# Kernel tuning notes

Measured on AMD Instinct MI355X. Metric: run time of the kernel, lower is better.

The kernel has to match this reference:

```python
import jax, jax.numpy as jnp
import numpy as np

N = 100_000
E = 1_600_000
D_IN, D_H, D_L = 128, 64, 32


def _glorot(key, shape):
    fan_in, fan_out = shape[0], shape[1]
    s = jnp.sqrt(6.0 / (fan_in + fan_out)).astype(jnp.float32)
    return jax.random.uniform(key, shape, jnp.float32, -s, s)


def setup_inputs() -> dict:
    key = jax.random.key(0)
    ks = jax.random.split(key, 8)
    x = jax.random.normal(ks[0], (N, D_IN), jnp.float32)
    edge_index = jax.random.randint(ks[1], (2, E), 0, N, dtype=jnp.int64)
    return {
        "x": x,
        "edge_index": edge_index,
        "W1": _glorot(ks[2], (D_IN, D_H)),
        "b1": jnp.zeros((D_H,), jnp.float32),
        "W2": _glorot(ks[3], (D_H, D_L)),
        "b2": jnp.zeros((D_L,), jnp.float32),
        "Wd1": _glorot(ks[4], (D_L, D_H)),
        "bd1": jnp.zeros((D_H,), jnp.float32),
        "Wd2": _glorot(ks[5], (D_H, D_IN)),
        "bd2": jnp.zeros((D_IN,), jnp.float32),
    }


def gcn_conv(x, W, b, src, dst, num_nodes):
    """PyG GCNConv: add self-loops, symmetric normalization, aggregate, bias."""
    loop = jnp.arange(num_nodes, dtype=src.dtype)
    s = jnp.concatenate([src, loop])  # sources (message senders)
    d = jnp.concatenate([dst, loop])  # targets (message receivers)
    deg = jax.ops.segment_sum(jnp.ones_like(s, dtype=x.dtype), d, num_segments=num_nodes)
    dinv = jnp.where(deg > 0, jax.lax.rsqrt(deg), 0.0)
    norm = dinv[s] * dinv[d]                      # [E+N]
    h = x @ W                                     # [N, out] dense transform first
    msgs = h[s] * norm[:, None]                   # gather + scale, [E+N, out]
    out = jax.ops.segment_sum(msgs, d, num_segments=num_nodes)  # scatter-add
    return out + b


def reference(x, edge_index, W1, b1, W2, b2, Wd1, bd1, Wd2, bd2):
    src, dst = edge_index[0], edge_index[1]
    n = x.shape[0]
    z = gcn_conv(x, W1, b1, src, dst, n)
    z = jax.nn.relu(z)
    z = gcn_conv(z, W2, b2, src, dst, n)          # latent embedding
    h = jax.nn.relu(z @ Wd1 + bd1)
    reconstructed_x = h @ Wd2 + bd2
    return (reconstructed_x, z)
```

## Files before the change

kernel.cpp:

```cpp
#include <hip/hip_runtime.h>
#include <stdint.h>

#define N_NODES 100000
#define N_EDGES 1600000
#define D_INF   128
#define D_HID   64
#define D_LAT   32
#define NB      98

typedef __attribute__((ext_vector_type(8))) short bf16x8;
typedef __attribute__((ext_vector_type(4))) float f32x4;

__device__ __forceinline__ unsigned short f2bf(float v) {
  union { float f; unsigned int u; } x; x.f = v;
  unsigned int u = x.u + 0x7FFF + ((x.u >> 16) & 1);
  return (unsigned short)(u >> 16);
}
__device__ __forceinline__ float bf2f(unsigned short h) {
  union { unsigned int u; float f; } x; x.u = ((unsigned int)h) << 16;
  return x.f;
}


#define NBKT      196
#define BKT_SHIFT 9
#define BKT_CAP   10240
#define EPB       4096
#define ABLOCKS   391
#define SPLITB    4

__global__ void k_zerobkt(int* __restrict__ bkcnt) {
  int t = threadIdx.x;
  if (t < NBKT) bkcnt[t] = 0;
}

__global__ __launch_bounds__(256) void k_binA(const int* __restrict__ esrc,
                                              const int* __restrict__ edst,
                                              int* __restrict__ bkcnt,
                                              int2* __restrict__ stage) {
  __shared__ int cnt[NBKT];
  __shared__ int sc[256];
  __shared__ int garel[NBKT];
  __shared__ int pos[NBKT];
  __shared__ __align__(16) int2 stg[EPB];
  __shared__ int gaddr[EPB];
  int t = threadIdx.x;
  int e0 = blockIdx.x * EPB;

  for (int i = t; i < NBKT; i += 256) cnt[i] = 0;
  __syncthreads();

  int ds[16], ss[16];
  const int4* s4 = (const int4*)esrc;
  const int4* d4 = (const int4*)edst;
#pragma unroll
  for (int i = 0; i < 4; i++) {
    int idx4 = (e0 >> 2) + i * 256 + t;
    int4 dd = make_int4(-1, -1, -1, -1);
    int4 sv = make_int4(0, 0, 0, 0);
    if (idx4 < N_EDGES / 4) { dd = d4[idx4]; sv = s4[idx4]; }
    ds[i*4+0] = dd.x; ds[i*4+1] = dd.y; ds[i*4+2] = dd.z; ds[i*4+3] = dd.w;
    ss[i*4+0] = sv.x; ss[i*4+1] = sv.y; ss[i*4+2] = sv.z; ss[i*4+3] = sv.w;
  }
#pragma unroll
  for (int j = 0; j < 16; j++)
    if (ds[j] >= 0) atomicAdd(&cnt[ds[j] >> BKT_SHIFT], 1);
  __syncthreads();

  int c = (t < NBKT) ? cnt[t] : 0;
  sc[t] = c;
  __syncthreads();
  int incl = c;
#pragma unroll
  for (int off = 1; off < 256; off <<= 1) {
    int x = (t >= off) ? sc[t - off] : 0;
    __syncthreads();
    incl += x;
    sc[t] = incl;
    __syncthreads();
  }
  if (t < NBKT) {
    int lb = incl - c;
    int gb = 0;
    if (c > 0) gb = t * BKT_CAP + atomicAdd(&bkcnt[t], c);
    garel[t] = gb - lb;
    pos[t]   = lb;
  }
  __syncthreads();

#pragma unroll
  for (int j = 0; j < 16; j++) {
    if (ds[j] >= 0) {
      int b  = ds[j] >> BKT_SHIFT;
      int lp = atomicAdd(&pos[b], 1);
      stg[lp]   = make_int2(ss[j], ds[j]);
      gaddr[lp] = garel[b] + lp;
    }
  }
  __syncthreads();

  int nval = N_EDGES - e0; if (nval > EPB) nval = EPB;
  for (int i = t; i < nval; i += 256)
    stage[gaddr[i]] = stg[i];
}

__global__ __launch_bounds__(256) void k_countB(const int2* __restrict__ stage,
                                                const int* __restrict__ bkcnt,
                                                int* __restrict__ counts) {
  __shared__ int hist[1 << BKT_SHIFT];
  int b = blockIdx.x;
  int t = threadIdx.x;
  for (int i = t; i < (1 << BKT_SHIFT); i += 256) hist[i] = 0;
  __syncthreads();
  int n = bkcnt[b];
  int nlo = b << BKT_SHIFT;
  const int2* reg = stage + (size_t)b * BKT_CAP;
  for (int i = t; i < n; i += 256)
    atomicAdd(&hist[reg[i].y - nlo], 1);
  __syncthreads();
  for (int i = t; i < (1 << BKT_SHIFT); i += 256) {
    int node = nlo + i;
    if (node < N_NODES) counts[node] = hist[i];
  }
}

__global__ void k_blocksum(const int* __restrict__ counts, int* __restrict__ bsums) {
  __shared__ int red[4];
  int base = blockIdx.x * 1024 + threadIdx.x * 4;
  int s = 0;
#pragma unroll
  for (int j = 0; j < 4; j++) { int i = base + j; if (i < N_NODES) s += counts[i]; }
#pragma unroll
  for (int off = 32; off > 0; off >>= 1) s += __shfl_down(s, off, 64);
  if ((threadIdx.x & 63) == 0) red[threadIdx.x >> 6] = s;
  __syncthreads();
  if (threadIdx.x == 0) bsums[blockIdx.x] = red[0] + red[1] + red[2] + red[3];
}

__global__ void k_scanblocks(const int* __restrict__ bsums, int* __restrict__ bbase,
                             int* __restrict__ offsets) {
  __shared__ int sh[128];
  int t = threadIdx.x;
  int v = (t < NB) ? bsums[t] : 0;
  sh[t] = v;
  __syncthreads();
  int incl = v;
#pragma unroll
  for (int off = 1; off < 128; off <<= 1) {
    int x = (t >= off) ? sh[t - off] : 0;
    __syncthreads();
    incl += x;
    sh[t] = incl;
    __syncthreads();
  }
  if (t < NB) bbase[t] = incl - v;
  if (t == NB - 1) offsets[N_NODES] = incl;
}

__global__ void k_scanchunk(const int* __restrict__ counts, const int* __restrict__ bbase,
                            int* __restrict__ offsets, int* __restrict__ cursor,
                            float* __restrict__ dinv) {
  __shared__ int sh[256];
  int b = blockIdx.x, t = threadIdx.x;
  int base = b * 1024 + t * 4;
  int v[4]; int s = 0;
#pragma unroll
  for (int j = 0; j < 4; j++) { v[j] = (base + j < N_NODES) ? counts[base + j] : 0; s += v[j]; }
  sh[t] = s;
  __syncthreads();
  int incl = s;
#pragma unroll
  for (int off = 1; off < 256; off <<= 1) {
    int x = (t >= off) ? sh[t - off] : 0;
    __syncthreads();
    incl += x;
    sh[t] = incl;
    __syncthreads();
  }
  int run = bbase[b] + incl - s;
#pragma unroll
  for (int j = 0; j < 4; j++) {
    int i = base + j;
    if (i < N_NODES) {
      offsets[i] = run;
      cursor[i]  = run;
      dinv[i]    = rsqrtf((float)(v[j] + 1));
      run += v[j];
    }
  }
}

__global__ __launch_bounds__(256) void k_binB(const int2* __restrict__ stage,
                                              const int* __restrict__ bkcnt,
                                              int* __restrict__ cursor,
                                              const float* __restrict__ dinv,
                                              int2* __restrict__ csr8) {
  int b   = blockIdx.x / SPLITB;
  int sub = blockIdx.x % SPLITB;
  int n = bkcnt[b];
  const int2* reg = stage + (size_t)b * BKT_CAP;
  for (int i = sub * 256 + threadIdx.x; i < n; i += SPLITB * 256) {
    int2 e = reg[i];
    int slot = atomicAdd(&cursor[e.y], 1);
    float w = dinv[e.x] * dinv[e.y];
    csr8[slot] = make_int2(e.x, __float_as_int(w));
  }
}


__global__ void k_prep_w(const float* __restrict__ W1, const float* __restrict__ W2,
                         const float* __restrict__ Wd1, const float* __restrict__ Wd2,
                         unsigned short* __restrict__ w1hi, unsigned short* __restrict__ w1lo,
                         unsigned short* __restrict__ w2hi, unsigned short* __restrict__ w2lo,
                         unsigned short* __restrict__ wd1hi, unsigned short* __restrict__ wd1lo,
                         unsigned short* __restrict__ wd2hi, unsigned short* __restrict__ wd2lo) {
  const float* src; unsigned short *hi, *lo; int K, M;
  switch (blockIdx.x) {
    case 0:  src = W1;  hi = w1hi;  lo = w1lo;  K = 128; M = 64;  break;
    case 1:  src = W2;  hi = w2hi;  lo = w2lo;  K = 64;  M = 32;  break;
    case 2:  src = Wd1; hi = wd1hi; lo = wd1lo; K = 32;  M = 64;  break;
    default: src = Wd2; hi = wd2hi; lo = wd2lo; K = 64;  M = 128; break;
  }
  int KP = K + 8;
  for (int i = threadIdx.x; i < K * M; i += 256) {
    int k = i / M, c = i % M;
    float v = src[i];
    unsigned short h = f2bf(v);
    hi[c * KP + k] = h;
    lo[c * KP + k] = f2bf(v - bf2f(h));
  }
}


template<int NODES, int K, int M>
__global__ __launch_bounds__(256) void k_mfma_gemm(const float* __restrict__ X,
                                                   const unsigned short* __restrict__ Bhi,
                                                   const unsigned short* __restrict__ Blo,
                                                   unsigned short* __restrict__ Y16) {
  constexpr int KP     = K + 8;
  constexpr int NSTRIP = M / 16;
  constexpr int KSTEPS = K / 32;
  constexpr int MTW    = (NODES / 16) * NSTRIP / 4;
  __shared__ __align__(16) unsigned short Ahi[NODES * KP];
  __shared__ __align__(16) unsigned short Alo[NODES * KP];

  int t = threadIdx.x;
  int node0 = blockIdx.x * NODES;

  for (int i = t; i < NODES * K / 4; i += 256) {
    int n = i / (K / 4), f4 = i % (K / 4);
    float4 v = make_float4(0.f, 0.f, 0.f, 0.f);
    if (node0 + n < N_NODES) v = ((const float4*)(X + (size_t)(node0 + n) * K))[f4];
    int base = n * KP + f4 * 4;
    float vv[4] = {v.x, v.y, v.z, v.w};
#pragma unroll
    for (int j = 0; j < 4; j++) {
      unsigned short h = f2bf(vv[j]);
      Ahi[base + j] = h;
      Alo[base + j] = f2bf(vv[j] - bf2f(h));
    }
  }
  __syncthreads();

  int w = t >> 6, lane = t & 63;
  int quad = lane >> 4, r16 = lane & 15;
  int strip = w % NSTRIP;

  bf16x8 bh[KSTEPS], bl[KSTEPS];
  const unsigned short* bp = Bhi + (strip * 16 + r16) * KP + quad * 8;
  const unsigned short* bq = Blo + (strip * 16 + r16) * KP + quad * 8;
#pragma unroll
  for (int ks = 0; ks < KSTEPS; ks++) {
    bh[ks] = *(const bf16x8*)(bp + ks * 32);
    bl[ks] = *(const bf16x8*)(bq + ks * 32);
  }

#pragma unroll
  for (int c = 0; c < MTW; c++) {
    int mt = (w / NSTRIP) * MTW + c;
    f32x4 acc = {0.f, 0.f, 0.f, 0.f};
    const unsigned short* ap = &Ahi[(mt * 16 + r16) * KP + quad * 8];
    const unsigned short* aq = &Alo[(mt * 16 + r16) * KP + quad * 8];
#pragma unroll
    for (int ks = 0; ks < KSTEPS; ks++) {
      bf16x8 ah = *(const bf16x8*)(ap + ks * 32);
      bf16x8 al = *(const bf16x8*)(aq + ks * 32);
      acc = __builtin_amdgcn_mfma_f32_16x16x32_bf16(ah, bh[ks], acc, 0, 0, 0);
      acc = __builtin_amdgcn_mfma_f32_16x16x32_bf16(ah, bl[ks], acc, 0, 0, 0);
      acc = __builtin_amdgcn_mfma_f32_16x16x32_bf16(al, bh[ks], acc, 0, 0, 0);
    }
    int gn  = node0 + mt * 16 + quad * 4;
    int col = strip * 16 + r16;
#pragma unroll
    for (int r = 0; r < 4; r++) {
      if (gn + r < N_NODES) Y16[(size_t)(gn + r) * M + col] = f2bf(acc[r]);
    }
  }
}


template<int FEAT, bool RELU>
__global__ __launch_bounds__(256) void k_aggregate(const unsigned short* __restrict__ H16,
                            const int* __restrict__ offsets,
                            const int2* __restrict__ csr8,
                            const float* __restrict__ dinv, const float* __restrict__ bias,
                            float* __restrict__ OUT) {
  constexpr int LPG    = FEAT / 4;
  constexpr int GROUPS = 64 / LPG;

  int node = blockIdx.x * 4 + (threadIdx.x >> 6);
  int lane = threadIdx.x & 63;
  if (node >= N_NODES) return;
  int beg = offsets[node], end = offsets[node + 1];
  int g  = lane / LPG;
  int f4 = lane % LPG;

  float a0 = 0.f, a1 = 0.f, a2 = 0.f, a3 = 0.f;

  int p = beg;
  for (; p + 2 * GROUPS <= end; p += 2 * GROUPS) {
    int2 e0 = csr8[p + g];
    int2 e1 = csr8[p + GROUPS + g];
    ushort4 h0 = *(const ushort4*)(H16 + (size_t)e0.x * FEAT + f4 * 4);
    ushort4 h1 = *(const ushort4*)(H16 + (size_t)e1.x * FEAT + f4 * 4);
    float w0 = __int_as_float(e0.y), w1 = __int_as_float(e1.y);
    a0 += bf2f(h0.x) * w0; a1 += bf2f(h0.y) * w0;
    a2 += bf2f(h0.z) * w0; a3 += bf2f(h0.w) * w0;
    a0 += bf2f(h1.x) * w1; a1 += bf2f(h1.y) * w1;
    a2 += bf2f(h1.z) * w1; a3 += bf2f(h1.w) * w1;
  }
  for (; p < end; p += GROUPS) {
    int q = p + g;
    int2 e = (q < end) ? csr8[q] : make_int2(node, 0);
    ushort4 h = *(const ushort4*)(H16 + (size_t)e.x * FEAT + f4 * 4);
    float w = __int_as_float(e.y);
    a0 += bf2f(h.x) * w; a1 += bf2f(h.y) * w;
    a2 += bf2f(h.z) * w; a3 += bf2f(h.w) * w;
  }

#pragma unroll
  for (int off = LPG; off < 64; off <<= 1) {
    a0 += __shfl_xor(a0, off, 64);
    a1 += __shfl_xor(a1, off, 64);
    a2 += __shfl_xor(a2, off, 64);
    a3 += __shfl_xor(a3, off, 64);
  }

  if (g == 0) {
    float di = dinv[node];
    float sw = di * di;
    ushort4 hs = *(const ushort4*)(H16 + (size_t)node * FEAT + f4 * 4);
    float4 bv = *(const float4*)(bias + f4 * 4);
    a0 += bf2f(hs.x) * sw + bv.x;
    a1 += bf2f(hs.y) * sw + bv.y;
    a2 += bf2f(hs.z) * sw + bv.z;
    a3 += bf2f(hs.w) * sw + bv.w;
    if (RELU) {
      a0 = fmaxf(a0, 0.f); a1 = fmaxf(a1, 0.f);
      a2 = fmaxf(a2, 0.f); a3 = fmaxf(a3, 0.f);
    }
    float4 o; o.x = a0; o.y = a1; o.z = a2; o.w = a3;
    *(float4*)(OUT + (size_t)node * FEAT + f4 * 4) = o;
  }
}


__global__ __launch_bounds__(256) void k_decoder_mfma(
    const float* __restrict__ Z,
    const unsigned short* __restrict__ B1hi, const unsigned short* __restrict__ B1lo,
    const float* __restrict__ bd1,
    const unsigned short* __restrict__ B2hi, const unsigned short* __restrict__ B2lo,
    const float* __restrict__ bd2, float* __restrict__ RECON) {
  constexpr int KP1 = 40;
  constexpr int KP2 = 72;
  __shared__ __align__(16) unsigned short Azhi[64 * KP1];
  __shared__ __align__(16) unsigned short Azlo[64 * KP1];
  __shared__ __align__(16) unsigned short H3hi[64 * KP2];
  __shared__ __align__(16) unsigned short H3lo[64 * KP2];
  int t = threadIdx.x;
  int node0 = blockIdx.x * 64;

  for (int i = t; i < 512; i += 256) {
    int n = i >> 3, f4 = i & 7;
    float4 v = make_float4(0.f, 0.f, 0.f, 0.f);
    if (node0 + n < N_NODES) v = ((const float4*)(Z + (size_t)(node0 + n) * 32))[f4];
    int base = n * KP1 + f4 * 4;
    float vv[4] = {v.x, v.y, v.z, v.w};
#pragma unroll
    for (int j = 0; j < 4; j++) {
      unsigned short h = f2bf(vv[j]);
      Azhi[base + j] = h;
      Azlo[base + j] = f2bf(vv[j] - bf2f(h));
    }
  }
  __syncthreads();

  int w = t >> 6, lane = t & 63;
  int quad = lane >> 4, r16 = lane & 15;

  {
    int col = w * 16 + r16;
    float bias1 = bd1[col];
    bf16x8 bh = *(const bf16x8*)(B1hi + col * KP1 + quad * 8);
    bf16x8 bl = *(const bf16x8*)(B1lo + col * KP1 + quad * 8);
#pragma unroll
    for (int m = 0; m < 4; m++) {
      bf16x8 ah = *(const bf16x8*)(Azhi + (m * 16 + r16) * KP1 + quad * 8);
      bf16x8 al = *(const bf16x8*)(Azlo + (m * 16 + r16) * KP1 + quad * 8);
      f32x4 acc = {0.f, 0.f, 0.f, 0.f};
      acc = __builtin_amdgcn_mfma_f32_16x16x32_bf16(ah, bh, acc, 0, 0, 0);
      acc = __builtin_amdgcn_mfma_f32_16x16x32_bf16(ah, bl, acc, 0, 0, 0);
      acc = __builtin_amdgcn_mfma_f32_16x16x32_bf16(al, bh, acc, 0, 0, 0);
#pragma unroll
      for (int r = 0; r < 4; r++) {
        int row = m * 16 + quad * 4 + r;
        float hv = fmaxf(acc[r] + bias1, 0.f);
        unsigned short h = f2bf(hv);
        H3hi[row * KP2 + col] = h;
        H3lo[row * KP2 + col] = f2bf(hv - bf2f(h));
      }
    }
  }
  __syncthreads();

#pragma unroll
  for (int sp = 0; sp < 2; sp++) {
    int strip = w + sp * 4;
    int col = strip * 16 + r16;
    float bias2 = bd2[col];
    const unsigned short* b2h = B2hi + col * KP2 + quad * 8;
    const unsigned short* b2l = B2lo + col * KP2 + quad * 8;
    bf16x8 bh0 = *(const bf16x8*)(b2h);
    bf16x8 bh1 = *(const bf16x8*)(b2h + 32);
    bf16x8 bl0 = *(const bf16x8*)(b2l);
    bf16x8 bl1 = *(const bf16x8*)(b2l + 32);
#pragma unroll
    for (int m = 0; m < 4; m++) {
      const unsigned short* ahp = H3hi + (m * 16 + r16) * KP2 + quad * 8;
      const unsigned short* alp = H3lo + (m * 16 + r16) * KP2 + quad * 8;
      bf16x8 ah0 = *(const bf16x8*)(ahp);
      bf16x8 ah1 = *(const bf16x8*)(ahp + 32);
      bf16x8 al0 = *(const bf16x8*)(alp);
      bf16x8 al1 = *(const bf16x8*)(alp + 32);
      f32x4 acc = {0.f, 0.f, 0.f, 0.f};
      acc = __builtin_amdgcn_mfma_f32_16x16x32_bf16(ah0, bh0, acc, 0, 0, 0);
      acc = __builtin_amdgcn_mfma_f32_16x16x32_bf16(ah1, bh1, acc, 0, 0, 0);
      acc = __builtin_amdgcn_mfma_f32_16x16x32_bf16(ah0, bl0, acc, 0, 0, 0);
      acc = __builtin_amdgcn_mfma_f32_16x16x32_bf16(ah1, bl1, acc, 0, 0, 0);
      acc = __builtin_amdgcn_mfma_f32_16x16x32_bf16(al0, bh0, acc, 0, 0, 0);
      acc = __builtin_amdgcn_mfma_f32_16x16x32_bf16(al1, bh1, acc, 0, 0, 0);
#pragma unroll
      for (int r = 0; r < 4; r++) {
        int n = node0 + m * 16 + quad * 4 + r;
        if (n < N_NODES) RECON[(size_t)n * 128 + col] = acc[r] + bias2;
      }
    }
  }
}


extern "C" void kernel_launch(void* const* d_in, const int* in_sizes, int n_in,
                              void* d_out, int out_size, void* d_ws, size_t ws_size,
                              hipStream_t stream) {
  const float* x    = (const float*)d_in[0];
  const int*   eidx = (const int*)d_in[1];
  const int*   esrc = eidx;
  const int*   edst = eidx + N_EDGES;
  const float* W1  = (const float*)d_in[2];
  const float* b1  = (const float*)d_in[3];
  const float* W2  = (const float*)d_in[4];
  const float* b2  = (const float*)d_in[5];
  const float* Wd1 = (const float*)d_in[6];
  const float* bd1 = (const float*)d_in[7];
  const float* Wd2 = (const float*)d_in[8];
  const float* bd2 = (const float*)d_in[9];

  float* recon = (float*)d_out;
  float* z     = (float*)d_out + (size_t)N_NODES * D_INF;
  int2*           stage = (int2*)recon;
  unsigned short* h1_16 = (unsigned short*)recon;
  float*          z1    = (float*)((char*)recon + 12800000);
  unsigned short* h2_16 = (unsigned short*)((char*)recon + 38400000);

  char* ws = (char*)d_ws;
  int*   counts  = (int*)(ws + 0);
  int*   offsets = (int*)(ws + 409600);
  int*   cursor  = (int*)(ws + 819200);
  float* dinv    = (float*)(ws + 1228800);
  int*   bsums   = (int*)(ws + 1638400);
  int*   bbase   = (int*)(ws + 1639424);
  int2*  csr8    = (int2*)(ws + 1640448);
  unsigned short* w1hi  = (unsigned short*)(ws + 14440448);
  unsigned short* w1lo  = (unsigned short*)(ws + 14457856);
  unsigned short* w2hi  = (unsigned short*)(ws + 14475264);
  unsigned short* w2lo  = (unsigned short*)(ws + 14479872);
  unsigned short* wd1hi = (unsigned short*)(ws + 14484480);
  unsigned short* wd1lo = (unsigned short*)(ws + 14489600);
  unsigned short* wd2hi = (unsigned short*)(ws + 14494720);
  unsigned short* wd2lo = (unsigned short*)(ws + 14513152);
  int*   bkcnt  = (int*)(ws + 14531584);

  k_zerobkt<<<1, 256, 0, stream>>>(bkcnt);
  k_binA<<<ABLOCKS, 256, 0, stream>>>(esrc, edst, bkcnt, stage);
  k_countB<<<NBKT, 256, 0, stream>>>(stage, bkcnt, counts);
  k_blocksum<<<NB, 256, 0, stream>>>(counts, bsums);
  k_scanblocks<<<1, 128, 0, stream>>>(bsums, bbase, offsets);
  k_scanchunk<<<NB, 256, 0, stream>>>(counts, bbase, offsets, cursor, dinv);
  k_binB<<<NBKT * SPLITB, 256, 0, stream>>>(stage, bkcnt, cursor, dinv, csr8);
  k_prep_w<<<4, 256, 0, stream>>>(W1, W2, Wd1, Wd2, w1hi, w1lo, w2hi, w2lo,
                                  wd1hi, wd1lo, wd2hi, wd2lo);

  k_mfma_gemm<64, 128, 64><<<(N_NODES + 63) / 64, 256, 0, stream>>>(x, w1hi, w1lo, h1_16);
  k_aggregate<64, true><<<(N_NODES + 3) / 4, 256, 0, stream>>>(h1_16, offsets, csr8, dinv, b1, z1);
  k_mfma_gemm<64, 64, 32><<<(N_NODES + 63) / 64, 256, 0, stream>>>(z1, w2hi, w2lo, h2_16);
  k_aggregate<32, false><<<(N_NODES + 3) / 4, 256, 0, stream>>>(h2_16, offsets, csr8, dinv, b2, z);
  k_decoder_mfma<<<(N_NODES + 63) / 64, 256, 0, stream>>>(z, wd1hi, wd1lo, bd1,
                                                          wd2hi, wd2lo, bd2, recon);
}
```

Baseline: 344.8 us.

## Split degree counting across blocks and widen aggregate loads to 8 bf16

```diff
diff --git a/kernel.cpp b/kernel.cpp
--- a/kernel.cpp
+++ b/kernel.cpp
@@ -10,6 +10,7 @@
 
 typedef __attribute__((ext_vector_type(8))) short bf16x8;
 typedef __attribute__((ext_vector_type(4))) float f32x4;
+typedef __attribute__((ext_vector_type(8))) unsigned short u16x8;
 
 __device__ __forceinline__ unsigned short f2bf(float v) {
   union { float f; unsigned int u; } x; x.f = v;
@@ -28,10 +29,12 @@
 #define EPB       4096
 #define ABLOCKS   391
 #define SPLITB    4
-
-__global__ void k_zerobkt(int* __restrict__ bkcnt) {
-  int t = threadIdx.x;
-  if (t < NBKT) bkcnt[t] = 0;
+#define SPLITC    4
+
+__global__ void k_zeroinit(int* __restrict__ counts, int* __restrict__ bkcnt) {
+  int i = blockIdx.x * 256 + threadIdx.x;
+  if (i < N_NODES) counts[i] = 0;
+  if (blockIdx.x == 0 && threadIdx.x < NBKT) bkcnt[threadIdx.x] = 0;
 }
 
 __global__ __launch_bounds__(256) void k_binA(const int* __restrict__ esrc,
@@ -108,19 +111,23 @@
                                                 const int* __restrict__ bkcnt,
                                                 int* __restrict__ counts) {
   __shared__ int hist[1 << BKT_SHIFT];
-  int b = blockIdx.x;
+  int b   = blockIdx.x / SPLITC;
+  int sub = blockIdx.x % SPLITC;
   int t = threadIdx.x;
   for (int i = t; i < (1 << BKT_SHIFT); i += 256) hist[i] = 0;
   __syncthreads();
   int n = bkcnt[b];
   int nlo = b << BKT_SHIFT;
   const int2* reg = stage + (size_t)b * BKT_CAP;
-  for (int i = t; i < n; i += 256)
+  for (int i = sub * 256 + t; i < n; i += SPLITC * 256)
     atomicAdd(&hist[reg[i].y - nlo], 1);
   __syncthreads();
   for (int i = t; i < (1 << BKT_SHIFT); i += 256) {
     int node = nlo + i;
-    if (node < N_NODES) counts[node] = hist[i];
+    if (node < N_NODES) {
+      int v = hist[i];
+      if (v) atomicAdd(&counts[node], v);
+    }
   }
 }
 
@@ -305,62 +312,71 @@
                             const int2* __restrict__ csr8,
                             const float* __restrict__ dinv, const float* __restrict__ bias,
                             float* __restrict__ OUT) {
-  constexpr int LPG    = FEAT / 4;
-  constexpr int GROUPS = 64 / LPG;
+  constexpr int LPE    = FEAT / 8;
+  constexpr int GROUPS = 64 / LPE;
 
   int node = blockIdx.x * 4 + (threadIdx.x >> 6);
   int lane = threadIdx.x & 63;
   if (node >= N_NODES) return;
   int beg = offsets[node], end = offsets[node + 1];
-  int g  = lane / LPG;
-  int f4 = lane % LPG;
-
-  float a0 = 0.f, a1 = 0.f, a2 = 0.f, a3 = 0.f;
-
-  int p = beg;
-  for (; p + 2 * GROUPS <= end; p += 2 * GROUPS) {
-    int2 e0 = csr8[p + g];
-    int2 e1 = csr8[p + GROUPS + g];
-    ushort4 h0 = *(const ushort4*)(H16 + (size_t)e0.x * FEAT + f4 * 4);
-    ushort4 h1 = *(const ushort4*)(H16 + (size_t)e1.x * FEAT + f4 * 4);
+  int g  = lane / LPE;
+  int f8 = lane % LPE;
+
+  float a0=0.f,a1=0.f,a2=0.f,a3=0.f,a4=0.f,a5=0.f,a6=0.f,a7=0.f;
+
+  for (int p = beg; p < end; p += 2 * GROUPS) {
+    int q0 = p + g, q1 = p + GROUPS + g;
+    int2 e0 = (q0 < end) ? csr8[q0] : make_int2(node, 0);
+    int2 e1 = (q1 < end) ? csr8[q1] : make_int2(node, 0);
+    u16x8 h0 = *(const u16x8*)(H16 + (size_t)e0.x * FEAT + f8 * 8);
+    u16x8 h1 = *(const u16x8*)(H16 + (size_t)e1.x * FEAT + f8 * 8);
     float w0 = __int_as_float(e0.y), w1 = __int_as_float(e1.y);
-    a0 += bf2f(h0.x) * w0; a1 += bf2f(h0.y) * w0;
-    a2 += bf2f(h0.z) * w0; a3 += bf2f(h0.w) * w0;
-    a0 += bf2f(h1.x) * w1; a1 += bf2f(h1.y) * w1;
-    a2 += bf2f(h1.z) * w1; a3 += bf2f(h1.w) * w1;
-  }
-  for (; p < end; p += GROUPS) {
-    int q = p + g;
-    int2 e = (q < end) ? csr8[q] : make_int2(node, 0);
-    ushort4 h = *(const ushort4*)(H16 + (size_t)e.x * FEAT + f4 * 4);
-    float w = __int_as_float(e.y);
-    a0 += bf2f(h.x) * w; a1 += bf2f(h.y) * w;
-    a2 += bf2f(h.z) * w; a3 += bf2f(h.w) * w;
-  }
-
-#pragma unroll
-  for (int off = LPG; off < 64; off <<= 1) {
+    a0 += bf2f(h0[0]) * w0; a1 += bf2f(h0[1]) * w0;
+    a2 += bf2f(h0[2]) * w0; a3 += bf2f(h0[3]) * w0;
+    a4 += bf2f(h0[4]) * w0; a5 += bf2f(h0[5]) * w0;
+    a6 += bf2f(h0[6]) * w0; a7 += bf2f(h0[7]) * w0;
+    a0 += bf2f(h1[0]) * w1; a1 += bf2f(h1[1]) * w1;
+    a2 += bf2f(h1[2]) * w1; a3 += bf2f(h1[3]) * w1;
+    a4 += bf2f(h1[4]) * w1; a5 += bf2f(h1[5]) * w1;
+    a6 += bf2f(h1[6]) * w1; a7 += bf2f(h1[7]) * w1;
+  }
+
+#pragma unroll
+  for (int off = LPE; off < 64; off <<= 1) {
     a0 += __shfl_xor(a0, off, 64);
     a1 += __shfl_xor(a1, off, 64);
     a2 += __shfl_xor(a2, off, 64);
     a3 += __shfl_xor(a3, off, 64);
+    a4 += __shfl_xor(a4, off, 64);
+    a5 += __shfl_xor(a5, off, 64);
+    a6 += __shfl_xor(a6, off, 64);
+    a7 += __shfl_xor(a7, off, 64);
   }
 
   if (g == 0) {
     float di = dinv[node];
     float sw = di * di;
-    ushort4 hs = *(const ushort4*)(H16 + (size_t)node * FEAT + f4 * 4);
-    float4 bv = *(const float4*)(bias + f4 * 4);
-    a0 += bf2f(hs.x) * sw + bv.x;
-    a1 += bf2f(hs.y) * sw + bv.y;
-    a2 += bf2f(hs.z) * sw + bv.z;
-    a3 += bf2f(hs.w) * sw + bv.w;
+    u16x8 hs = *(const u16x8*)(H16 + (size_t)node * FEAT + f8 * 8);
+    float4 bv0 = *(const float4*)(bias + f8 * 8);
+    float4 bv1 = *(const float4*)(bias + f8 * 8 + 4);
+    a0 += bf2f(hs[0]) * sw + bv0.x;
+    a1 += bf2f(hs[1]) * sw + bv0.y;
+    a2 += bf2f(hs[2]) * sw + bv0.z;
+    a3 += bf2f(hs[3]) * sw + bv0.w;
+    a4 += bf2f(hs[4]) * sw + bv1.x;
+    a5 += bf2f(hs[5]) * sw + bv1.y;
+    a6 += bf2f(hs[6]) * sw + bv1.z;
+    a7 += bf2f(hs[7]) * sw + bv1.w;
     if (RELU) {
       a0 = fmaxf(a0, 0.f); a1 = fmaxf(a1, 0.f);
       a2 = fmaxf(a2, 0.f); a3 = fmaxf(a3, 0.f);
-    }
-    float4 o; o.x = a0; o.y = a1; o.z = a2; o.w = a3;
-    *(float4*)(OUT + (size_t)node * FEAT + f4 * 4) = o;
+      a4 = fmaxf(a4, 0.f); a5 = fmaxf(a5, 0.f);
+      a6 = fmaxf(a6, 0.f); a7 = fmaxf(a7, 0.f);
+    }
+    float4 o0; o0.x = a0; o0.y = a1; o0.z = a2; o0.w = a3;
+    float4 o1; o1.x = a4; o1.y = a5; o1.z = a6; o1.w = a7;
+    *(float4*)(OUT + (size_t)node * FEAT + f8 * 8)     = o0;
+    *(float4*)(OUT + (size_t)node * FEAT + f8 * 8 + 4) = o1;
   }
 }
 
@@ -500,9 +516,9 @@
   unsigned short* wd2lo = (unsigned short*)(ws + 14513152);
   int*   bkcnt  = (int*)(ws + 14531584);
 
-  k_zerobkt<<<1, 256, 0, stream>>>(bkcnt);
+  k_zeroinit<<<391, 256, 0, stream>>>(counts, bkcnt);
   k_binA<<<ABLOCKS, 256, 0, stream>>>(esrc, edst, bkcnt, stage);
-  k_countB<<<NBKT, 256, 0, stream>>>(stage, bkcnt, counts);
+  k_countB<<<NBKT * SPLITC, 256, 0, stream>>>(stage, bkcnt, counts);
   k_blocksum<<<NB, 256, 0, stream>>>(counts, bsums);
   k_scanblocks<<<1, 128, 0, stream>>>(bsums, bbase, offsets);
   k_scanchunk<<<NB, 256, 0, stream>>>(counts, bbase, offsets, cursor, dinv);
```

Result: faster. 324.7 us (-5.8%).
